# Performance work log

Measured on AMD Instinct MI355X. Metric: run time of the kernel, lower is better.

The kernel has to match this reference:

```python
import jax, jax.numpy as jnp
import numpy as np

HOP = 768
NCB = 14
DIM = 512
VOCAB = 1024
W_SCALE = 0.02  # keep conv stacks numerically tame


def conv1d(x, w, b, stride=1, padding=0):
    # x: [B,C,L], w: [O,I,K] (torch layout), b: [O]
    y = jax.lax.conv_general_dilated(
        x, w, window_strides=(stride,), padding=[(padding, padding)],
        dimension_numbers=('NCH', 'OIH', 'NCH'))
    return y + b[None, :, None]


def conv_transpose1d(x, w, b, stride, padding):
    # torch ConvTranspose1d weight layout: (in, out, k)
    k = w.shape[2]
    w2 = jnp.flip(jnp.transpose(w, (1, 0, 2)), axis=2)  # -> OIH
    y = jax.lax.conv_general_dilated(
        x, w2, window_strides=(1,),
        padding=[(k - 1 - padding, k - 1 - padding)],
        lhs_dilation=(stride,),
        dimension_numbers=('NCH', 'OIH', 'NCH'))
    return y + b[None, :, None]


def setup_inputs() -> dict:
    key = jax.random.key(0)
    ks = jax.random.split(key, 16)
    f = lambda k, shp, s=W_SCALE: jax.random.normal(k, shp, dtype=jnp.float32) * s
    B, T = 2, 98304  # T = 768 * 128
    return {
        'audio': jax.random.normal(ks[0], (B, 1, T), dtype=jnp.float32),
        'codebooks': jax.random.normal(ks[1], (NCB, VOCAB, DIM), dtype=jnp.float32),
        'ew1': f(ks[2], (256, 1, 7)), 'eb1': f(ks[3], (256,)),
        'ew2': f(ks[4], (512, 256, 5)), 'eb2': f(ks[5], (512,)),
        'ew3': f(ks[6], (NCB * DIM, 512, 3)), 'eb3': f(ks[7], (NCB * DIM,)),
        'dw1': f(ks[8], (NCB * DIM, 512, 5)), 'db1': f(ks[9], (512,)),
        'dw2': f(ks[10], (256, 512, 5)), 'db2': f(ks[11], (256,)),
        'dw3': f(ks[12], (1, 256, 7)), 'db3': f(ks[13], (1,)),
    }


def reference(audio, codebooks, ew1, eb1, ew2, eb2, ew3, eb3,
              dw1, db1, dw2, db2, dw3, db3):
    B = audio.shape[0]
    # ---- encoder ----
    h = jax.nn.relu(conv1d(audio, ew1, eb1, stride=1, padding=3))
    h = jax.nn.relu(conv1d(h, ew2, eb2, stride=HOP, padding=2))
    h = conv1d(h, ew3, eb3, stride=1, padding=1)          # [B, NCB*DIM, S]
    S = h.shape[-1]
    emb = h.reshape(B, NCB, DIM, S).transpose(0, 1, 3, 2)  # [B, NCB, S, DIM]
    # ---- VQ: per-codebook squared L2 distance + argmin (same argmin as cdist) ----
    d2 = (jnp.sum(emb * emb, axis=-1, keepdims=True)            # [B,NCB,S,1]
          - 2.0 * jnp.einsum('bksd,kvd->bksv', emb, codebooks)  # [B,NCB,S,V]
          + jnp.sum(codebooks * codebooks, axis=-1)[None, :, None, :])
    codes = jnp.argmin(d2, axis=-1)                        # [B, NCB, S] int
    # ---- decode: embedding lookup + transposed conv decoder ----
    q = codebooks[jnp.arange(NCB)[None, :, None], codes]   # [B, NCB, S, DIM]
    q = q.transpose(0, 1, 3, 2).reshape(B, NCB * DIM, S)   # [B, NCB*DIM, S]
    a = jax.nn.relu(conv_transpose1d(q, dw1, db1, stride=HOP, padding=2))
    a = jax.nn.relu(conv1d(a, dw2, db2, stride=1, padding=2))
    a = jnp.tanh(conv1d(a, dw3, db3, stride=1, padding=3))
    return a  # [B, 1, (S-1)*HOP + 1]
```

## Files before the change

kernel.cpp:

```cpp
#include <hip/hip_runtime.h>
#include <hip/hip_bf16.h>
#include <math.h>

#define T_IN 98304
#define SS 128
#define NBATCH 2
#define NN 256
#define C1 256
#define C2 512
#define C3 7168
#define NCBK 14
#define DIMV 512
#define VOC 1024
#define TOUT 97537
#define HOP 768

#define OFF_CBN    0L
#define OFF_AB1    14336L
#define OFF_AB2    14848L
#define OFF_CCONST 15104L
#define OFF_H2C    15120L
#define OFF_H2XH   146192L
#define OFF_H2XL   342800L
#define OFF_H3H    539408L
#define OFF_H3L    1456912L
#define OFF_SCORES 2374416L
#define OFF_X1H    2374416L
#define OFF_X1L    2538256L
#define OFF_DW1T   539408L
#define OFF_XH     539408L
#define OFF_XL     3488528L
#define OFF_CODES  9714448L
#define OFF_QBF    9718032L
#define OFF_A1RAW  10635536L
#define OFF_A2ACT  11290896L

typedef __attribute__((ext_vector_type(8))) short short8;
typedef __attribute__((ext_vector_type(4))) float f32x4;

static __device__ inline ushort f2bf(float x) {
  __hip_bfloat16 h = __float2bfloat16(x);
  return *reinterpret_cast<ushort*>(&h);
}

static __device__ inline void split8(const float4 x0, const float4 x1,
                                     short8& h, short8& l) {
  float xs[8] = {x0.x, x0.y, x0.z, x0.w, x1.x, x1.y, x1.z, x1.w};
  #pragma unroll
  for (int e = 0; e < 8; ++e) {
    uint b = __float_as_uint(xs[e]);
    h[e] = (short)(b >> 16);
    float r = xs[e] - __uint_as_float(b & 0xffff0000u);
    l[e] = (short)(__float_as_uint(r) >> 16);
  }
}

__global__ void k_cbn(const float* __restrict__ cb, float* __restrict__ cbn) {
  int row = blockIdx.x * 4 + (threadIdx.x >> 6);
  int lane = threadIdx.x & 63;
  const float* p = cb + (long)row * DIMV;
  float s = 0.f;
  for (int d = lane; d < DIMV; d += 64) { float x = p[d]; s += x * x; }
  for (int off = 32; off; off >>= 1) s += __shfl_down(s, off);
  if (lane == 0) cbn[row] = s;
}

__global__ __launch_bounds__(256) void k_prep_ab2(const float* __restrict__ db1,
    const float* __restrict__ dw2, const float* __restrict__ db2,
    float* __restrict__ ab1, float* __restrict__ ab2) {
  __shared__ float red[256];
  int o = blockIdx.x, t = threadIdx.x;
  if (o == 0) { ab1[t] = fmaxf(db1[t], 0.f); ab1[t + 256] = fmaxf(db1[t + 256], 0.f); }
  const float* wp = dw2 + (long)o * C2 * 5;
  float acc = 0.f;
  #pragma unroll
  for (int h = 0; h < 2; ++h) {
    int c = t + h * 256;
    const float* p = wp + c * 5;
    float wsum = p[0] + p[1] + p[2] + p[3] + p[4];
    acc = fmaf(wsum, fmaxf(db1[c], 0.f), acc);
  }
  red[t] = acc;
  __syncthreads();
  for (int off = 128; off; off >>= 1) {
    if (t < off) red[t] += red[t + off];
    __syncthreads();
  }
  if (t == 0) ab2[o] = fmaxf(red[0] + db2[o], 0.f);
}

__global__ __launch_bounds__(256) void k_prep_c(const float* __restrict__ dw3,
    const float* __restrict__ db3, const float* __restrict__ ab2,
    float* __restrict__ cconst) {
  __shared__ float red[256];
  int t = threadIdx.x;
  float wsum3 = 0.f;
  #pragma unroll
  for (int j = 0; j < 7; ++j) wsum3 += dw3[t*7+j];
  red[t] = wsum3 * ab2[t];
  __syncthreads();
  for (int off = 128; off; off >>= 1) {
    if (t < off) red[t] += red[t + off];
    __syncthreads();
  }
  if (t == 0) cconst[0] = tanhf(red[0] + db3[0]);
}

__global__ __launch_bounds__(256) void k_enc1(const float* __restrict__ audio,
    const float* __restrict__ ew1, const float* __restrict__ eb1,
    ushort* __restrict__ X1h, ushort* __restrict__ X1l) {
  int n = blockIdx.x, ic = threadIdx.x;
  int b = n >> 7, s = n & 127;
  const float* ap = audio + (long)b * T_IN;
  int base = HOP * s - 5;
  float a[11];
  #pragma unroll
  for (int w = 0; w < 11; ++w) {
    int ai = base + w;
    a[w] = (ai >= 0 && ai < T_IN) ? ap[ai] : 0.f;
  }
  float w1[7];
  #pragma unroll
  for (int j = 0; j < 7; ++j) w1[j] = ew1[ic*7+j];
  float b1 = eb1[ic];
  long off = (long)n * 1280 + ic * 5;
  #pragma unroll
  for (int jj = 0; jj < 5; ++jj) {
    int tcol = HOP * s + jj - 2;
    float v = 0.f;
    if (tcol >= 0) {
      float acc = b1;
      #pragma unroll
      for (int j = 0; j < 7; ++j) acc = fmaf(w1[j], a[jj + j], acc);
      v = fmaxf(acc, 0.f);
    }
    uint bi = __float_as_uint(v);
    X1h[off + jj] = (ushort)(bi >> 16);
    float r = v - __uint_as_float(bi & 0xffff0000u);
    X1l[off + jj] = (ushort)(__float_as_uint(r) >> 16);
  }
}

__global__ __launch_bounds__(256) void gemm_enc2(const float* __restrict__ ew2,
    const ushort* __restrict__ X1h, const ushort* __restrict__ X1l,
    const float* __restrict__ eb2, float* __restrict__ h2c) {
  __shared__ __align__(16) float red[4 * 2048];
  const int tid = threadIdx.x;
  const int w = tid >> 6, lane = tid & 63;
  const int l15 = lane & 15, quad = lane >> 4;
  const int m0 = blockIdx.x * 32, n0 = blockIdx.y * 64;
  const int kbase = w * 320;
  f32x4 acc[2][4] = {};
  const float*  aB = ew2 + (long)(m0 + l15) * 1280 + kbase + quad * 8;
  const ushort* bhB = X1h + (long)(n0 + l15) * 1280 + kbase + quad * 8;
  const ushort* blB = X1l + (long)(n0 + l15) * 1280 + kbase + quad * 8;
  for (int k0 = 0; k0 < 320; k0 += 32) {
    short8 ah[2], al[2], bh[4], bl[4];
    #pragma unroll
    for (int f = 0; f < 2; ++f) {
      const float* ap = aB + (long)f * 16 * 1280 + k0;
      float4 x0 = *(const float4*)ap;
      float4 x1 = *(const float4*)(ap + 4);
      split8(x0, x1, ah[f], al[f]);
    }
    #pragma unroll
    for (int f = 0; f < 4; ++f) {
      bh[f] = *(const short8*)(bhB + (long)f * 16 * 1280 + k0);
      bl[f] = *(const short8*)(blB + (long)f * 16 * 1280 + k0);
    }
    #pragma unroll
    for (int i = 0; i < 2; ++i)
      #pragma unroll
      for (int j = 0; j < 4; ++j) {
        acc[i][j] = __builtin_amdgcn_mfma_f32_16x16x32_bf16(ah[i], bh[j], acc[i][j], 0, 0, 0);
        acc[i][j] = __builtin_amdgcn_mfma_f32_16x16x32_bf16(ah[i], bl[j], acc[i][j], 0, 0, 0);
        acc[i][j] = __builtin_amdgcn_mfma_f32_16x16x32_bf16(al[i], bh[j], acc[i][j], 0, 0, 0);
      }
  }
  #pragma unroll
  for (int i = 0; i < 2; ++i)
    #pragma unroll
    for (int j = 0; j < 4; ++j)
      *(float4*)&red[w * 2048 + (i * 4 + j) * 256 + lane * 4] = *(float4*)&acc[i][j];
  __syncthreads();
  #pragma unroll
  for (int q = 0; q < 2; ++q) {
    const int c = 2 * w + q;
    const int i = c >> 2, j = c & 3;
    float4 s = make_float4(0.f, 0.f, 0.f, 0.f);
    #pragma unroll
    for (int g = 0; g < 4; ++g) {
      float4 t4 = *(const float4*)&red[g * 2048 + c * 256 + lane * 4];
      s.x += t4.x; s.y += t4.y; s.z += t4.z; s.w += t4.w;
    }
    const int obase = m0 + i * 16 + quad * 4;
    float4 bias = *(const float4*)(eb2 + obase);
    const int n = n0 + j * 16 + l15;
    float4 out;
    out.x = fmaxf(s.x + bias.x, 0.f);
    out.y = fmaxf(s.y + bias.y, 0.f);
    out.z = fmaxf(s.z + bias.z, 0.f);
    out.w = fmaxf(s.w + bias.w, 0.f);
    *(float4*)(h2c + (long)n * C2 + obase) = out;
  }
}

__global__ void k_h2x(const float* __restrict__ h2c, ushort* __restrict__ h2xh,
                      ushort* __restrict__ h2xl) {
  int idx = blockIdx.x * 256 + threadIdx.x;
  const int total = NN * 1536;
  for (; idx < total; idx += gridDim.x * 256) {
    int n = idx / 1536, r = idx - n * 1536;
    int ic = r / 3, j = r - ic * 3;
    int s2 = (n & 127) + j - 1;
    int b = n >> 7;
    float v = (s2 >= 0 && s2 < SS) ? h2c[(long)(b*SS + s2)*C2 + ic] : 0.f;
    uint bi = __float_as_uint(v);
    h2xh[idx] = (ushort)(bi >> 16);
    float rr = v - __uint_as_float(bi & 0xffff0000u);
    h2xl[idx] = (ushort)(__float_as_uint(rr) >> 16);
  }
}

__global__ __launch_bounds__(256) void gemm_h3(const float* __restrict__ A,
    const ushort* __restrict__ Bh, const ushort* __restrict__ Bl,
    const float* __restrict__ eb3, ushort* __restrict__ h3h, ushort* __restrict__ h3l) {
  __shared__ __align__(16) float red[4 * 4096];
  const int tid = threadIdx.x;
  const int w = tid >> 6, lane = tid & 63;
  const int l15 = lane & 15, quad = lane >> 4;
  const int m0 = blockIdx.x * 64, n0 = blockIdx.y * 64;
  const int kbase = w * 384;
  f32x4 acc[4][4] = {};
  const float*  aB = A  + (long)(m0 + l15) * 1536 + kbase + quad * 8;
  const ushort* bhB = Bh + (long)(n0 + l15) * 1536 + kbase + quad * 8;
  const ushort* blB = Bl + (long)(n0 + l15) * 1536 + kbase + quad * 8;
  for (int k0 = 0; k0 < 384; k0 += 32) {
    short8 ah[4], al[4], bh[4], bl[4];
    #pragma unroll
    for (int f = 0; f < 4; ++f) {
      const float* ap = aB + (long)f * 16 * 1536 + k0;
      float4 x0 = *(const float4*)ap;
      float4 x1 = *(const float4*)(ap + 4);
      split8(x0, x1, ah[f], al[f]);
      bh[f] = *(const short8*)(bhB + (long)f * 16 * 1536 + k0);
      bl[f] = *(const short8*)(blB + (long)f * 16 * 1536 + k0);
    }
    #pragma unroll
    for (int i = 0; i < 4; ++i)
      #pragma unroll
      for (int j = 0; j < 4; ++j) {
        acc[i][j] = __builtin_amdgcn_mfma_f32_16x16x32_bf16(ah[i], bh[j], acc[i][j], 0, 0, 0);
        acc[i][j] = __builtin_amdgcn_mfma_f32_16x16x32_bf16(ah[i], bl[j], acc[i][j], 0, 0, 0);
        acc[i][j] = __builtin_amdgcn_mfma_f32_16x16x32_bf16(al[i], bh[j], acc[i][j], 0, 0, 0);
      }
  }
  #pragma unroll
  for (int i = 0; i < 4; ++i)
    #pragma unroll
    for (int j = 0; j < 4; ++j)
      *(float4*)&red[w * 4096 + (i * 4 + j) * 256 + lane * 4] = *(float4*)&acc[i][j];
  __syncthreads();
  const int mbase = m0 + w * 16 + quad * 4;
  float4 bias = *(const float4*)(eb3 + mbase);
  #pragma unroll
  for (int j = 0; j < 4; ++j) {
    float4 s = *(const float4*)&red[(w * 4 + j) * 256 + lane * 4];
    #pragma unroll
    for (int r = 1; r < 4; ++r) {
      float4 tt = *(const float4*)&red[r * 4096 + (w * 4 + j) * 256 + lane * 4];
      s.x += tt.x; s.y += tt.y; s.z += tt.z; s.w += tt.w;
    }
    const int n = n0 + j * 16 + l15;
    float v0 = s.x + bias.x;
    float v1 = s.y + bias.y;
    float v2 = s.z + bias.z;
    float v3 = s.w + bias.w;
    uint b0 = __float_as_uint(v0), b1 = __float_as_uint(v1);
    uint b2 = __float_as_uint(v2), b3 = __float_as_uint(v3);
    uint2 hp;
    hp.x = (b0 >> 16) | (b1 & 0xffff0000u);
    hp.y = (b2 >> 16) | (b3 & 0xffff0000u);
    float r0 = v0 - __uint_as_float(b0 & 0xffff0000u);
    float r1 = v1 - __uint_as_float(b1 & 0xffff0000u);
    float r2 = v2 - __uint_as_float(b2 & 0xffff0000u);
    float r3 = v3 - __uint_as_float(b3 & 0xffff0000u);
    uint2 lp;
    lp.x = (__float_as_uint(r0) >> 16) | (__float_as_uint(r1) & 0xffff0000u);
    lp.y = (__float_as_uint(r2) >> 16) | (__float_as_uint(r3) & 0xffff0000u);
    long off = (long)n * C3 + mbase;
    *(uint2*)(h3h + off) = hp;
    *(uint2*)(h3l + off) = lp;
  }
}

__global__ __launch_bounds__(256) void gemm_scores(const float* __restrict__ cb,
    const ushort* __restrict__ h3h, const ushort* __restrict__ h3l,
    const float* __restrict__ cbn, float* __restrict__ scores) {
  __shared__ __align__(16) float red[4 * 4096];
  const int tid = threadIdx.x;
  const int w = tid >> 6, lane = tid & 63;
  const int l15 = lane & 15, quad = lane >> 4;
  const int m0 = blockIdx.x * 64, n0 = blockIdx.y * 64, z = blockIdx.z;
  const int kbase = w * 128;
  f32x4 acc[4][4] = {};
  const float*  aB = cb + (long)z * VOC * DIMV + (long)(m0 + l15) * 512 + kbase + quad * 8;
  const ushort* bhB = h3h + (long)(n0 + l15) * C3 + z * 512 + kbase + quad * 8;
  const ushort* blB = h3l + (long)(n0 + l15) * C3 + z * 512 + kbase + quad * 8;
  for (int k0 = 0; k0 < 128; k0 += 32) {
    short8 ah[4], al[4], bh[4], bl[4];
    #pragma unroll
    for (int f = 0; f < 4; ++f) {
      const float* ap = aB + (long)f * 16 * 512 + k0;
      float4 x0 = *(const float4*)ap;
      float4 x1 = *(const float4*)(ap + 4);
      split8(x0, x1, ah[f], al[f]);
      bh[f] = *(const short8*)(bhB + (long)f * 16 * C3 + k0);
      bl[f] = *(const short8*)(blB + (long)f * 16 * C3 + k0);
    }
    #pragma unroll
    for (int i = 0; i < 4; ++i)
      #pragma unroll
      for (int j = 0; j < 4; ++j) {
        acc[i][j] = __builtin_amdgcn_mfma_f32_16x16x32_bf16(ah[i], bh[j], acc[i][j], 0, 0, 0);
        acc[i][j] = __builtin_amdgcn_mfma_f32_16x16x32_bf16(ah[i], bl[j], acc[i][j], 0, 0, 0);
        acc[i][j] = __builtin_amdgcn_mfma_f32_16x16x32_bf16(al[i], bh[j], acc[i][j], 0, 0, 0);
      }
  }
  #pragma unroll
  for (int i = 0; i < 4; ++i)
    #pragma unroll
    for (int j = 0; j < 4; ++j)
      *(float4*)&red[w * 4096 + (i * 4 + j) * 256 + lane * 4] = *(float4*)&acc[i][j];
  __syncthreads();
  const int vbase = m0 + w * 16 + quad * 4;
  float4 cn = *(const float4*)(cbn + z * VOC + vbase);
  #pragma unroll
  for (int j = 0; j < 4; ++j) {
    float4 s = *(const float4*)&red[(w * 4 + j) * 256 + lane * 4];
    #pragma unroll
    for (int r = 1; r < 4; ++r) {
      float4 tt = *(const float4*)&red[r * 4096 + (w * 4 + j) * 256 + lane * 4];
      s.x += tt.x; s.y += tt.y; s.z += tt.z; s.w += tt.w;
    }
    const int n = n0 + j * 16 + l15;
    float4 out;
    out.x = cn.x - 2.f * s.x;
    out.y = cn.y - 2.f * s.y;
    out.z = cn.z - 2.f * s.z;
    out.w = cn.w - 2.f * s.w;
    *(float4*)(scores + ((long)z * NN + n) * VOC + vbase) = out;
  }
}

__global__ void k_argmin(const float* __restrict__ scores, int* __restrict__ codes) {
  int row = blockIdx.x;
  int lane = threadIdx.x;
  const float* p = scores + (long)row * VOC;
  float best = 3.4e38f; int bi = 0;
  for (int i = 0; i < 16; ++i) {
    int v = i * 64 + lane;
    float x = p[v];
    if (x < best) { best = x; bi = v; }
  }
  for (int off = 32; off; off >>= 1) {
    float ob = __shfl_down(best, off);
    int oi = __shfl_down(bi, off);
    if (ob < best || (ob == best && oi < bi)) { best = ob; bi = oi; }
  }
  if (lane == 0) codes[row] = bi;
}

__global__ __launch_bounds__(256) void k_dw1t(const float* __restrict__ dw1,
                                              ushort* __restrict__ dw1p) {
  __shared__ __align__(16) ushort T[64 * 72];
  int t = threadIdx.x;
  int k0 = blockIdx.x * 64, m0 = blockIdx.y * 64;
  int kk = t >> 2, mj = (t & 3) * 16;
  const float* src = dw1 + (long)(k0 + kk) * 2560 + m0 + mj;
  float x[16];
  *(float4*)&x[0]  = *(const float4*)(src);
  *(float4*)&x[4]  = *(const float4*)(src + 4);
  *(float4*)&x[8]  = *(const float4*)(src + 8);
  *(float4*)&x[12] = *(const float4*)(src + 12);
  #pragma unroll
  for (int l = 0; l < 16; ++l)
    T[(mj + l) * 72 + kk] = f2bf(x[l]);
  __syncthreads();
  int mo = t >> 2, kc = (t & 3) * 16;
  const int m = m0 + mo;
  const int mt = m >> 4, l15 = m & 15;
  #pragma unroll
  for (int h = 0; h < 2; ++h) {
    const int kk0 = kc + h * 8;
    const int kglob = k0 + kk0;
    const int kt = kglob >> 5;
    const int quad = (kglob >> 3) & 3;
    uint4 u = *(const uint4*)&T[mo * 72 + kk0];
    *(uint4*)(dw1p + ((long)(mt * 224 + kt)) * 512 + (quad * 16 + l15) * 8) = u;
  }
}

__global__ void k_gather_qbf(const float* __restrict__ cb, const int* __restrict__ codes,
                             ushort* __restrict__ qp) {
  int o = blockIdx.x * 256 + threadIdx.x;
  const int total = NN * C3 / 8;
  if (o >= total) return;
  int frag = o >> 6, r = o & 63;
  int quad = r >> 4, l15 = r & 15;
  int nt = frag / 224, kt = frag - nt * 224;
  int n = nt * 16 + l15;
  int kglob = kt * 32 + quad * 8;
  int kcb = kglob >> 9, d0 = kglob & 511;
  int code = codes[kcb * NN + n];
  const float* s = cb + ((long)(kcb * VOC + code)) * DIMV + d0;
  float4 x0 = *(const float4*)s;
  float4 x1 = *(const float4*)(s + 4);
  uint4 u;
  u.x = (uint)f2bf(x0.x) | ((uint)f2bf(x0.y) << 16);
  u.y = (uint)f2bf(x0.z) | ((uint)f2bf(x0.w) << 16);
  u.z = (uint)f2bf(x1.x) | ((uint)f2bf(x1.y) << 16);
  u.w = (uint)f2bf(x1.z) | ((uint)f2bf(x1.w) << 16);
  ((uint4*)qp)[o] = u;
}

__global__ __launch_bounds__(1024) void gemm_a1_mfma(const ushort* __restrict__ dw1p,
    const ushort* __restrict__ qp, float* __restrict__ a1raw) {
  __shared__ __align__(16) float red[4 * 4096];
  const int tid = threadIdx.x;
  const int w = tid >> 6, lane = tid & 63;
  const int l15 = lane & 15, quad = lane >> 4;
  const int mt0 = blockIdx.x * 4, nt0 = blockIdx.y * 4;
  const int kt0 = w * 14;
  f32x4 acc[4][4] = {};
  const ushort* aB = dw1p + ((long)(mt0 * 224 + kt0)) * 512 + lane * 8;
  const ushort* bB = qp   + ((long)(nt0 * 224 + kt0)) * 512 + lane * 8;
  #pragma unroll 2
  for (int kt = 0; kt < 14; ++kt) {
    short8 ah[4], bh[4];
    #pragma unroll
    for (int f = 0; f < 4; ++f) {
      ah[f] = *(const short8*)(aB + ((long)(f * 224 + kt)) * 512);
      bh[f] = *(const short8*)(bB + ((long)(f * 224 + kt)) * 512);
    }
    #pragma unroll
    for (int i = 0; i < 4; ++i)
      #pragma unroll
      for (int j = 0; j < 4; ++j)
        acc[i][j] = __builtin_amdgcn_mfma_f32_16x16x32_bf16(ah[i], bh[j], acc[i][j], 0, 0, 0);
  }
  float4 rsum = make_float4(0.f, 0.f, 0.f, 0.f);
  #pragma unroll
  for (int r = 0; r < 4; ++r) {
    if ((w >> 2) == r) {
      #pragma unroll
      for (int i = 0; i < 4; ++i)
        #pragma unroll
        for (int j = 0; j < 4; ++j)
          *(float4*)&red[(w & 3) * 4096 + (i * 4 + j) * 256 + lane * 4] = *(float4*)&acc[i][j];
    }
    __syncthreads();
    #pragma unroll
    for (int g = 0; g < 4; ++g) {
      float4 t4 = *(const float4*)&red[g * 4096 + w * 256 + lane * 4];
      rsum.x += t4.x; rsum.y += t4.y; rsum.z += t4.z; rsum.w += t4.w;
    }
    __syncthreads();
  }
  const int ci = w >> 2, cj = w & 3;
  const int n = nt0 * 16 + cj * 16 + l15;
  const int mb = mt0 * 16 + ci * 16 + quad * 4;
  float v[4] = {rsum.x, rsum.y, rsum.z, rsum.w};
  #pragma unroll
  for (int reg = 0; reg < 4; ++reg) {
    int m = mb + reg;
    int c = m / 5, jj = m - c * 5;
    a1raw[((long)(n * 5 + jj)) * C2 + c] = v[reg];
  }
}

__global__ void k_x2(const float* __restrict__ a1raw, const float* __restrict__ ab1g,
                     const float* __restrict__ db1, ushort* __restrict__ Xh,
                     ushort* __restrict__ Xl) {
  int idx = blockIdx.x * 256 + threadIdx.x;
  const int total = 2304 * 2560;
  for (; idx < total; idx += gridDim.x * 256) {
    int nu = idx / 2560, ck = idx - nu * 2560;
    int n = nu / 9, u = nu - n * 9;
    int c = ck / 5, jj = ck - c * 5;
    int w = u + jj;
    int s = n & 127;
    int tc = HOP * s - 6 + w;
    float v;
    if (tc < 0 || tc > TOUT - 1) v = 0.f;
    else if (w >= 4 && w <= 8)
      v = fmaxf(db1[c] + a1raw[((long)(n * 5 + (w - 4))) * C2 + c], 0.f);
    else v = ab1g[c];
    uint bi = __float_as_uint(v);
    Xh[idx] = (ushort)(bi >> 16);
    float rr = v - __uint_as_float(bi & 0xffff0000u);
    Xl[idx] = (ushort)(__float_as_uint(rr) >> 16);
  }
}

__global__ __launch_bounds__(256) void gemm_dec2(const float* __restrict__ dw2,
    const ushort* __restrict__ Xh, const ushort* __restrict__ Xl,
    const float* __restrict__ db2, float* __restrict__ a2act) {
  __shared__ __align__(16) float red[4 * 4096];
  const int tid = threadIdx.x;
  const int w = tid >> 6, lane = tid & 63;
  const int l15 = lane & 15, quad = lane >> 4;
  const int m0 = blockIdx.x * 64, n0 = blockIdx.y * 64;
  const int kbase = w * 640;
  f32x4 acc[4][4] = {};
  const float*  aB = dw2 + (long)(m0 + l15) * 2560 + kbase + quad * 8;
  const ushort* bhB = Xh + (long)(n0 + l15) * 2560 + kbase + quad * 8;
  const ushort* blB = Xl + (long)(n0 + l15) * 2560 + kbase + quad * 8;
  for (int k0 = 0; k0 < 640; k0 += 32) {
    short8 ah[4], al[4], bh[4], bl[4];
    #pragma unroll
    for (int f = 0; f < 4; ++f) {
      const float* ap = aB + (long)f * 16 * 2560 + k0;
      float4 x0 = *(const float4*)ap;
      float4 x1 = *(const float4*)(ap + 4);
      split8(x0, x1, ah[f], al[f]);
      bh[f] = *(const short8*)(bhB + (long)f * 16 * 2560 + k0);
      bl[f] = *(const short8*)(blB + (long)f * 16 * 2560 + k0);
    }
    #pragma unroll
    for (int i = 0; i < 4; ++i)
      #pragma unroll
      for (int j = 0; j < 4; ++j) {
        acc[i][j] = __builtin_amdgcn_mfma_f32_16x16x32_bf16(ah[i], bh[j], acc[i][j], 0, 0, 0);
        acc[i][j] = __builtin_amdgcn_mfma_f32_16x16x32_bf16(ah[i], bl[j], acc[i][j], 0, 0, 0);
        acc[i][j] = __builtin_amdgcn_mfma_f32_16x16x32_bf16(al[i], bh[j], acc[i][j], 0, 0, 0);
      }
  }
  #pragma unroll
  for (int i = 0; i < 4; ++i)
    #pragma unroll
    for (int j = 0; j < 4; ++j)
      *(float4*)&red[w * 4096 + (i * 4 + j) * 256 + lane * 4] = *(float4*)&acc[i][j];
  __syncthreads();
  const int mb = m0 + w * 16 + quad * 4;
  float4 bias = *(const float4*)(db2 + mb);
  #pragma unroll
  for (int j = 0; j < 4; ++j) {
    float4 s = *(const float4*)&red[(w * 4 + j) * 256 + lane * 4];
    #pragma unroll
    for (int r = 1; r < 4; ++r) {
      float4 tt = *(const float4*)&red[r * 4096 + (w * 4 + j) * 256 + lane * 4];
      s.x += tt.x; s.y += tt.y; s.z += tt.z; s.w += tt.w;
    }
    const int nu = n0 + j * 16 + l15;
    float4 out;
    out.x = fmaxf(s.x + bias.x, 0.f);
    out.y = fmaxf(s.y + bias.y, 0.f);
    out.z = fmaxf(s.z + bias.z, 0.f);
    out.w = fmaxf(s.w + bias.w, 0.f);
    *(float4*)(a2act + (long)nu * C1 + mb) = out;
  }
}

__global__ void k_fill(float* __restrict__ outp, const float* __restrict__ cconst) {
  float v = cconst[0];
  int idx = blockIdx.x * 256 + threadIdx.x;
  const int total = NBATCH * TOUT;
  for (; idx < total; idx += gridDim.x * 256) outp[idx] = v;
}

__global__ __launch_bounds__(256) void k_dec3(const float* __restrict__ a2act,
    const float* __restrict__ ab2g, const float* __restrict__ dw3,
    const float* __restrict__ db3, float* __restrict__ outp) {
  __shared__ float sa2[9 * C1];
  __shared__ float sb[C1];
  int n = blockIdx.x;
  int s = n & 127, b = n >> 7;
  int t = threadIdx.x;
  for (int i = t; i < 9 * C1; i += 256) sa2[i] = a2act[(long)n * 9 * C1 + i];
  sb[t] = ab2g[t];
  __syncthreads();
  int wv = t >> 6, lane = t & 63;
  float b3 = db3[0];
  for (int w15 = wv; w15 < 15; w15 += 4) {
    int tc = HOP * s - 7 + w15;
    if (tc < 0 || tc > TOUT - 1) continue;
    float part = 0.f;
    for (int cc = lane; cc < C1; cc += 64) {
      #pragma unroll
      for (int j = 0; j < 7; ++j) {
        int wcol = tc + j - 3;
        float x;
        if (wcol < 0 || wcol > TOUT - 1) x = 0.f;
        else {
          int du = wcol - (HOP * s - 4);
          x = (du >= 0 && du <= 8) ? sa2[du * C1 + cc] : sb[cc];
        }
        part = fmaf(dw3[cc*7+j], x, part);
      }
    }
    for (int off = 32; off; off >>= 1) part += __shfl_down(part, off);
    if (lane == 0) outp[(long)b * TOUT + tc] = tanhf(part + b3);
  }
}

extern "C" void kernel_launch(void* const* d_in, const int* in_sizes, int n_in,
                              void* d_out, int out_size, void* d_ws, size_t ws_size,
                              hipStream_t stream) {
  const float* audio = (const float*)d_in[0];
  const float* cb    = (const float*)d_in[1];
  const float* ew1   = (const float*)d_in[2];
  const float* eb1   = (const float*)d_in[3];
  const float* ew2   = (const float*)d_in[4];
  const float* eb2   = (const float*)d_in[5];
  const float* ew3   = (const float*)d_in[6];
  const float* eb3   = (const float*)d_in[7];
  const float* dw1   = (const float*)d_in[8];
  const float* db1   = (const float*)d_in[9];
  const float* dw2   = (const float*)d_in[10];
  const float* db2   = (const float*)d_in[11];
  const float* dw3   = (const float*)d_in[12];
  const float* db3   = (const float*)d_in[13];
  float* outp = (float*)d_out;
  float* ws = (float*)d_ws;

  float*  cbn    = ws + OFF_CBN;
  float*  ab1    = ws + OFF_AB1;
  float*  ab2    = ws + OFF_AB2;
  float*  cconst = ws + OFF_CCONST;
  float*  h2c    = ws + OFF_H2C;
  ushort* h2xh   = (ushort*)(ws + OFF_H2XH);
  ushort* h2xl   = (ushort*)(ws + OFF_H2XL);
  ushort* h3h    = (ushort*)(ws + OFF_H3H);
  ushort* h3l    = (ushort*)(ws + OFF_H3L);
  float*  scores = ws + OFF_SCORES;
  ushort* X1h    = (ushort*)(ws + OFF_X1H);
  ushort* X1l    = (ushort*)(ws + OFF_X1L);
  ushort* dw1p   = (ushort*)(ws + OFF_DW1T);
  ushort* Xh     = (ushort*)(ws + OFF_XH);
  ushort* Xl     = (ushort*)(ws + OFF_XL);
  int*    codes  = (int*)(ws + OFF_CODES);
  ushort* qp     = (ushort*)(ws + OFF_QBF);
  float*  a1raw  = ws + OFF_A1RAW;
  float*  a2act  = ws + OFF_A2ACT;

  k_cbn<<<3584, 256, 0, stream>>>(cb, cbn);
  k_prep_ab2<<<C1, 256, 0, stream>>>(db1, dw2, db2, ab1, ab2);
  k_prep_c<<<1, 256, 0, stream>>>(dw3, db3, ab2, cconst);
  k_enc1<<<NN, 256, 0, stream>>>(audio, ew1, eb1, X1h, X1l);
  gemm_enc2<<<dim3(16, 4), 256, 0, stream>>>(ew2, X1h, X1l, eb2, h2c);
  k_h2x<<<384, 256, 0, stream>>>(h2c, h2xh, h2xl);
  gemm_h3<<<dim3(112, 4), 256, 0, stream>>>(ew3, h2xh, h2xl, eb3, h3h, h3l);
  gemm_scores<<<dim3(16, 4, 14), 256, 0, stream>>>(cb, h3h, h3l, cbn, scores);
  k_argmin<<<NCBK * NN, 64, 0, stream>>>(scores, codes);
  k_dw1t<<<dim3(112, 40), 256, 0, stream>>>(dw1, dw1p);
  k_gather_qbf<<<896, 256, 0, stream>>>(cb, codes, qp);
  gemm_a1_mfma<<<dim3(40, 4), 1024, 0, stream>>>(dw1p, qp, a1raw);
  k_x2<<<4096, 256, 0, stream>>>(a1raw, ab1, db1, Xh, Xl);
  gemm_dec2<<<dim3(4, 36), 256, 0, stream>>>(dw2, Xh, Xl, db2, a2act);
  k_fill<<<256, 256, 0, stream>>>(outp, cconst);
  k_dec3<<<NN, 256, 0, stream>>>(a2act, ab2, dw3, db3, outp);
}
```

Baseline: 410.3 us.

## Pre-pack ew3 and activations into MFMA fragment layout for gemm_h3

Adds a kernel that splits ew3 into bf16 hi/lo parts and stores them in per-lane MFMA fragment order, processed in two halves to fit the workspace. h2x and the h3 output are also written in fragment-packed order, so gemm_h3 and gemm_scores read contiguous short8 per lane instead of strided rows. gemm_h3 uses a 1D grid with an XCD-aware block mapping. This trades an extra pass that writes the ~22 MB weight into packed form, and two extra launches, for coalesced loads and no on-the-fly float splitting in the GEMM.

```diff
diff --git a/kernel.cpp b/kernel.cpp
--- a/kernel.cpp
+++ b/kernel.cpp
@@ -27,6 +27,8 @@
 #define OFF_SCORES 2374416L
 #define OFF_X1H    2374416L
 #define OFF_X1L    2538256L
+#define OFF_EW3PH  2374416L
+#define OFF_EW3PL  5126928L
 #define OFF_DW1T   539408L
 #define OFF_XH     539408L
 #define OFF_XL     3488528L
@@ -205,46 +207,77 @@
   }
 }
 
-__global__ void k_h2x(const float* __restrict__ h2c, ushort* __restrict__ h2xh,
-                      ushort* __restrict__ h2xl) {
+__global__ void k_h2x(const float* __restrict__ h2c, ushort* __restrict__ h2xph,
+                      ushort* __restrict__ h2xpl) {
   int idx = blockIdx.x * 256 + threadIdx.x;
   const int total = NN * 1536;
   for (; idx < total; idx += gridDim.x * 256) {
-    int n = idx / 1536, r = idx - n * 1536;
-    int ic = r / 3, j = r - ic * 3;
+    int grp = idx >> 9;
+    int r = idx & 511;
+    int e = r & 7, lane = r >> 3;
+    int quad = lane >> 4, l15 = lane & 15;
+    int nt = grp / 48, kt = grp - nt * 48;
+    int n = nt * 16 + l15;
+    int k = kt * 32 + quad * 8 + e;
+    int ic = k / 3, j = k - ic * 3;
     int s2 = (n & 127) + j - 1;
     int b = n >> 7;
     float v = (s2 >= 0 && s2 < SS) ? h2c[(long)(b*SS + s2)*C2 + ic] : 0.f;
     uint bi = __float_as_uint(v);
-    h2xh[idx] = (ushort)(bi >> 16);
+    h2xph[idx] = (ushort)(bi >> 16);
     float rr = v - __uint_as_float(bi & 0xffff0000u);
-    h2xl[idx] = (ushort)(__float_as_uint(rr) >> 16);
-  }
-}
-
-__global__ __launch_bounds__(256) void gemm_h3(const float* __restrict__ A,
-    const ushort* __restrict__ Bh, const ushort* __restrict__ Bl,
-    const float* __restrict__ eb3, ushort* __restrict__ h3h, ushort* __restrict__ h3l) {
+    h2xpl[idx] = (ushort)(__float_as_uint(rr) >> 16);
+  }
+}
+
+__global__ __launch_bounds__(256) void k_ew3p(const float* __restrict__ ew3,
+    ushort* __restrict__ ph, ushort* __restrict__ pl, int mrow0) {
+  int o8 = blockIdx.x * 256 + threadIdx.x;
+  const int total = 3584 * 1536 / 8;
+  if (o8 >= total) return;
+  int frag = o8 >> 6, lane = o8 & 63;
+  int quad = lane >> 4, l15 = lane & 15;
+  int mtL = frag / 48, kt = frag - mtL * 48;
+  int m = mrow0 + mtL * 16 + l15;
+  int k = kt * 32 + quad * 8;
+  const float* s = ew3 + (long)m * 1536 + k;
+  float4 x0 = *(const float4*)s;
+  float4 x1 = *(const float4*)(s + 4);
+  short8 h, l;
+  split8(x0, x1, h, l);
+  long off = (long)o8 * 8;
+  *(short8*)(ph + off) = h;
+  *(short8*)(pl + off) = l;
+}
+
+__global__ __launch_bounds__(256) void gemm_h3(const ushort* __restrict__ aH,
+    const ushort* __restrict__ aL, const ushort* __restrict__ bH,
+    const ushort* __restrict__ bL, const float* __restrict__ eb3,
+    ushort* __restrict__ h3ph, ushort* __restrict__ h3pl, int mrow0) {
   __shared__ __align__(16) float red[4 * 4096];
   const int tid = threadIdx.x;
   const int w = tid >> 6, lane = tid & 63;
   const int l15 = lane & 15, quad = lane >> 4;
-  const int m0 = blockIdx.x * 64, n0 = blockIdx.y * 64;
-  const int kbase = w * 384;
+  const int bid = blockIdx.x;
+  const int xcd = bid & 7, q = bid >> 3;
+  const int mchunk = xcd * 7 + (q >> 2);
+  const int nchunk = q & 3;
+  const int mtL0 = mchunk * 4, nt0 = nchunk * 4, n0 = nchunk * 64;
+  const int kt0 = w * 12;
   f32x4 acc[4][4] = {};
-  const float*  aB = A  + (long)(m0 + l15) * 1536 + kbase + quad * 8;
-  const ushort* bhB = Bh + (long)(n0 + l15) * 1536 + kbase + quad * 8;
-  const ushort* blB = Bl + (long)(n0 + l15) * 1536 + kbase + quad * 8;
-  for (int k0 = 0; k0 < 384; k0 += 32) {
+  const ushort* aHB = aH + ((long)(mtL0 * 48 + kt0)) * 512 + lane * 8;
+  const ushort* aLB = aL + ((long)(mtL0 * 48 + kt0)) * 512 + lane * 8;
+  const ushort* bHB = bH + ((long)(nt0 * 48 + kt0)) * 512 + lane * 8;
+  const ushort* bLB = bL + ((long)(nt0 * 48 + kt0)) * 512 + lane * 8;
+  for (int kt = 0; kt < 12; ++kt) {
     short8 ah[4], al[4], bh[4], bl[4];
     #pragma unroll
     for (int f = 0; f < 4; ++f) {
-      const float* ap = aB + (long)f * 16 * 1536 + k0;
-      float4 x0 = *(const float4*)ap;
-      float4 x1 = *(const float4*)(ap + 4);
-      split8(x0, x1, ah[f], al[f]);
-      bh[f] = *(const short8*)(bhB + (long)f * 16 * 1536 + k0);
-      bl[f] = *(const short8*)(blB + (long)f * 16 * 1536 + k0);
+      long o = ((long)(f * 48 + kt)) * 512;
+      ah[f] = *(const short8*)(aHB + o);
+      al[f] = *(const short8*)(aLB + o);
+      bh[f] = *(const short8*)(bHB + o);
+      bl[f] = *(const short8*)(bLB + o);
     }
     #pragma unroll
     for (int i = 0; i < 4; ++i)
@@ -261,8 +294,9 @@
     for (int j = 0; j < 4; ++j)
       *(float4*)&red[w * 4096 + (i * 4 + j) * 256 + lane * 4] = *(float4*)&acc[i][j];
   __syncthreads();
-  const int mbase = m0 + w * 16 + quad * 4;
-  float4 bias = *(const float4*)(eb3 + mbase);
+  const int mg0 = mrow0 + mchunk * 64 + w * 16 + quad * 4;
+  float4 bias = *(const float4*)(eb3 + mg0);
+  const int ktS = mg0 >> 5, quadk = (mg0 >> 3) & 3, es = mg0 & 7;
   #pragma unroll
   for (int j = 0; j < 4; ++j) {
     float4 s = *(const float4*)&red[(w * 4 + j) * 256 + lane * 4];
@@ -288,14 +322,14 @@
     uint2 lp;
     lp.x = (__float_as_uint(r0) >> 16) | (__float_as_uint(r1) & 0xffff0000u);
     lp.y = (__float_as_uint(r2) >> 16) | (__float_as_uint(r3) & 0xffff0000u);
-    long off = (long)n * C3 + mbase;
-    *(uint2*)(h3h + off) = hp;
-    *(uint2*)(h3l + off) = lp;
+    long off = ((long)((n >> 4) * 224 + ktS)) * 512 + (quadk * 16 + (n & 15)) * 8 + es;
+    *(uint2*)(h3ph + off) = hp;
+    *(uint2*)(h3pl + off) = lp;
   }
 }
 
 __global__ __launch_bounds__(256) void gemm_scores(const float* __restrict__ cb,
-    const ushort* __restrict__ h3h, const ushort* __restrict__ h3l,
+    const ushort* __restrict__ h3ph, const ushort* __restrict__ h3pl,
     const float* __restrict__ cbn, float* __restrict__ scores) {
   __shared__ __align__(16) float red[4 * 4096];
   const int tid = threadIdx.x;
@@ -305,8 +339,8 @@
   const int kbase = w * 128;
   f32x4 acc[4][4] = {};
   const float*  aB = cb + (long)z * VOC * DIMV + (long)(m0 + l15) * 512 + kbase + quad * 8;
-  const ushort* bhB = h3h + (long)(n0 + l15) * C3 + z * 512 + kbase + quad * 8;
-  const ushort* blB = h3l + (long)(n0 + l15) * C3 + z * 512 + kbase + quad * 8;
+  const ushort* bHB = h3ph + ((long)((n0 >> 4) * 224 + z * 16 + (kbase >> 5))) * 512 + lane * 8;
+  const ushort* bLB = h3pl + ((long)((n0 >> 4) * 224 + z * 16 + (kbase >> 5))) * 512 + lane * 8;
   for (int k0 = 0; k0 < 128; k0 += 32) {
     short8 ah[4], al[4], bh[4], bl[4];
     #pragma unroll
@@ -315,8 +349,9 @@
       float4 x0 = *(const float4*)ap;
       float4 x1 = *(const float4*)(ap + 4);
       split8(x0, x1, ah[f], al[f]);
-      bh[f] = *(const short8*)(bhB + (long)f * 16 * C3 + k0);
-      bl[f] = *(const short8*)(blB + (long)f * 16 * C3 + k0);
+      long o = ((long)(f * 224) + (k0 >> 5)) * 512;
+      bh[f] = *(const short8*)(bHB + o);
+      bl[f] = *(const short8*)(bLB + o);
     }
     #pragma unroll
     for (int i = 0; i < 4; ++i)
@@ -629,13 +664,15 @@
   float*  ab2    = ws + OFF_AB2;
   float*  cconst = ws + OFF_CCONST;
   float*  h2c    = ws + OFF_H2C;
-  ushort* h2xh   = (ushort*)(ws + OFF_H2XH);
-  ushort* h2xl   = (ushort*)(ws + OFF_H2XL);
-  ushort* h3h    = (ushort*)(ws + OFF_H3H);
-  ushort* h3l    = (ushort*)(ws + OFF_H3L);
+  ushort* h2xph  = (ushort*)(ws + OFF_H2XH);
+  ushort* h2xpl  = (ushort*)(ws + OFF_H2XL);
+  ushort* h3ph   = (ushort*)(ws + OFF_H3H);
+  ushort* h3pl   = (ushort*)(ws + OFF_H3L);
   float*  scores = ws + OFF_SCORES;
   ushort* X1h    = (ushort*)(ws + OFF_X1H);
   ushort* X1l    = (ushort*)(ws + OFF_X1L);
+  ushort* ew3ph  = (ushort*)(ws + OFF_EW3PH);
+  ushort* ew3pl  = (ushort*)(ws + OFF_EW3PL);
   ushort* dw1p   = (ushort*)(ws + OFF_DW1T);
   ushort* Xh     = (ushort*)(ws + OFF_XH);
   ushort* Xl     = (ushort*)(ws + OFF_XL);
@@ -649,9 +686,12 @@
   k_prep_c<<<1, 256, 0, stream>>>(dw3, db3, ab2, cconst);
   k_enc1<<<NN, 256, 0, stream>>>(audio, ew1, eb1, X1h, X1l);
   gemm_enc2<<<dim3(16, 4), 256, 0, stream>>>(ew2, X1h, X1l, eb2, h2c);
-  k_h2x<<<384, 256, 0, stream>>>(h2c, h2xh, h2xl);
-  gemm_h3<<<dim3(112, 4), 256, 0, stream>>>(ew3, h2xh, h2xl, eb3, h3h, h3l);
-  gemm_scores<<<dim3(16, 4, 14), 256, 0, stream>>>(cb, h3h, h3l, cbn, scores);
+  k_h2x<<<384, 256, 0, stream>>>(h2c, h2xph, h2xpl);
+  k_ew3p<<<2688, 256, 0, stream>>>(ew3, ew3ph, ew3pl, 0);
+  gemm_h3<<<224, 256, 0, stream>>>(ew3ph, ew3pl, h2xph, h2xpl, eb3, h3ph, h3pl, 0);
+  k_ew3p<<<2688, 256, 0, stream>>>(ew3, ew3ph, ew3pl, 3584);
+  gemm_h3<<<224, 256, 0, stream>>>(ew3ph, ew3pl, h2xph, h2xpl, eb3, h3ph, h3pl, 3584);
+  gemm_scores<<<dim3(16, 4, 14), 256, 0, stream>>>(cb, h3ph, h3pl, cbn, scores);
   k_argmin<<<NCBK * NN, 64, 0, stream>>>(scores, codes);
   k_dw1t<<<dim3(112, 40), 256, 0, stream>>>(dw1, dw1p);
   k_gather_qbf<<<896, 256, 0, stream>>>(cb, codes, qp);
```

Result: slower. 419.5 us (+2.2%).
